# Kernel optimization log

Measured on AMD Instinct MI355X. Metric: run time of the kernel, lower is better.

## Reference

```python
import jax, jax.numpy as jnp
import numpy as np

N_NODES = 100000
N_EDGES = 1600000
D = 128
N_LAYERS = 4
N_GRAPHS = 512


def setup_inputs() -> dict:
    key = jax.random.key(0)
    ks = jax.random.split(key, 12)
    x = jax.random.normal(ks[0], (N_NODES, D), dtype=jnp.float32)
    edge_index = jax.random.randint(ks[1], (2, N_EDGES), 0, N_NODES, dtype=jnp.int64)
    batch = jnp.sort(jax.random.randint(ks[2], (N_NODES,), 0, N_GRAPHS, dtype=jnp.int64))
    scale = 1.0 / np.sqrt(D)
    Ws = jax.random.normal(ks[3], (N_LAYERS, D, D), dtype=jnp.float32) * scale
    bs = jnp.zeros((N_LAYERS, D), dtype=jnp.float32)
    mlp_w1 = jax.random.normal(ks[4], (D, 100), dtype=jnp.float32) * scale
    mlp_b1 = jnp.zeros((100,), dtype=jnp.float32)
    mlp_w2 = jax.random.normal(ks[5], (100, 4), dtype=jnp.float32) * (1.0 / np.sqrt(100.0))
    mlp_b2 = jnp.zeros((4,), dtype=jnp.float32)
    return {"x": x, "Ws": Ws, "bs": bs, "mlp_w1": mlp_w1, "mlp_b1": mlp_b1,
            "mlp_w2": mlp_w2, "mlp_b2": mlp_b2, "edge_index": edge_index, "batch": batch}


def _gcn_conv(x, W, b, row, col, norm):
    # x: [N, Din]; W: [Din, Dout]. PyG GCNConv: linear, then normalized scatter-add.
    xw = x @ W                                # [N, Dout]
    msg = xw[row] * norm[:, None]             # gather at source nodes [E', Dout]
    out = jax.ops.segment_sum(msg, col, num_segments=N_NODES)
    return out + b


def reference(x, Ws, bs, mlp_w1, mlp_b1, mlp_w2, mlp_b2, edge_index, batch):
    # Add self-loops and compute symmetric normalization (once; shared by all layers).
    loop = jnp.arange(N_NODES, dtype=edge_index.dtype)
    row = jnp.concatenate([edge_index[0], loop])  # source
    col = jnp.concatenate([edge_index[1], loop])  # target
    deg = jax.ops.segment_sum(jnp.ones_like(col, dtype=x.dtype), col, num_segments=N_NODES)
    dinv = jnp.where(deg > 0, jax.lax.rsqrt(deg), 0.0)
    norm = dinv[row] * dinv[col]              # [E']

    h = x
    for i in range(N_LAYERS - 1):
        # dropout is identity in eval mode
        h = _gcn_conv(h, Ws[i], bs[i], row, col, norm)
        h = jax.nn.relu(h)
    h = _gcn_conv(h, Ws[-1], bs[-1], row, col, norm)

    # global mean pool over graphs
    sums = jax.ops.segment_sum(h, batch, num_segments=N_GRAPHS)
    counts = jax.ops.segment_sum(jnp.ones((N_NODES,), dtype=h.dtype), batch, num_segments=N_GRAPHS)
    pooled = sums / jnp.maximum(counts, 1.0)[:, None]  # [G, D]

    # MLP head: D -> 100 -> 4 (relu between, dropout identity in eval)
    hid = jax.nn.relu(pooled @ mlp_w1 + mlp_b1)
    pred = hid @ mlp_w2 + mlp_b2
    return pred
```

## Files before the change

### kernel.cpp

```cpp
#include <hip/hip_runtime.h>

#define N_NODES  100000
#define N_EDGES  1600000
#define DIM      128
#define N_GRAPHS 512

#define BW       512
#define NBUCK    ((N_NODES + BW - 1) / BW)
#define CAP      12288
#define NB_CHUNK 4096

typedef short  bf16x8 __attribute__((ext_vector_type(8)));
typedef float  f32x4  __attribute__((ext_vector_type(4)));

__device__ inline ushort f2bf(float f) {
    union { float f; unsigned u; } v; v.f = f;
    unsigned r = v.u + 0x7FFFu + ((v.u >> 16) & 1u);
    return (ushort)(r >> 16);
}
__device__ inline float bf2f_lo(unsigned u) { union { unsigned u; float f; } v; v.u = u << 16; return v.f; }
__device__ inline float bf2f_hi(unsigned u) { union { unsigned u; float f; } v; v.u = u & 0xFFFF0000u; return v.f; }


__global__ __launch_bounds__(256) void cvt_x(const float* __restrict__ x,
                                             const float* __restrict__ dinv,
                                             ushort* __restrict__ xb) {
    int i = (blockIdx.x * 256 + threadIdx.x) * 4;
    float d = dinv[i >> 7];
    float4 v = *(const float4*)(x + i);
    ushort4 o;
    o.x = f2bf(v.x * d); o.y = f2bf(v.y * d); o.z = f2bf(v.z * d); o.w = f2bf(v.w * d);
    *(ushort4*)(xb + i) = o;
}

__global__ __launch_bounds__(256) void cvt_w(const float* __restrict__ Ws,
                                             ushort* __restrict__ WT) {
    int idx = blockIdx.x * 256 + threadIdx.x;
    int L = idx >> 14, n = (idx >> 7) & 127, k = idx & 127;
    WT[idx] = f2bf(Ws[(L << 14) + (k << 7) + n]);
}


__global__ __launch_bounds__(256) void initb_kernel(int* __restrict__ bfill,
                                                    int* __restrict__ csr) {
    int t = threadIdx.x;
    if (t < NBUCK) bfill[t] = t * CAP;
    if (t == 255) csr[N_NODES] = N_EDGES;
}

__global__ __launch_bounds__(1024) void bin_kernel(const int* __restrict__ row,
                                                   const int* __restrict__ col,
                                                   int* __restrict__ bfill,
                                                   unsigned* __restrict__ tmp) {
    __shared__ unsigned s_val[NB_CHUNK];
    __shared__ int s_dst[NB_CHUNK];
    __shared__ int s_hist[256], s_scan[256];
    __shared__ int s_excl[NBUCK], s_base[NBUCK], s_cur[NBUCK];
    int t = threadIdx.x;
    int e0 = blockIdx.x * NB_CHUNK;

    if (t < 256) s_hist[t] = 0;
    __syncthreads();
#pragma unroll
    for (int k = 0; k < 4; ++k) {
        int e = e0 + t + k * 1024;
        if (e < N_EDGES) atomicAdd(&s_hist[col[e] >> 9], 1);
    }
    __syncthreads();
    int h = 0;
    if (t < 256) { h = s_hist[t]; s_scan[t] = h; }
    __syncthreads();
    for (int o = 1; o < 256; o <<= 1) {
        int u = 0;
        if (t < 256 && t >= o) u = s_scan[t - o];
        __syncthreads();
        if (t < 256) s_scan[t] += u;
        __syncthreads();
    }
    if (t < NBUCK) {
        int ex = s_scan[t] - h;
        s_excl[t] = ex;
        s_cur[t]  = ex;
        s_base[t] = atomicAdd(&bfill[t], h);
    }
    __syncthreads();
#pragma unroll
    for (int k = 0; k < 4; ++k) {
        int e = e0 + t + k * 1024;
        if (e < N_EDGES) {
            int r = row[e], c = col[e];
            int b = c >> 9;
            int p = atomicAdd(&s_cur[b], 1);
            int dst = s_base[b] + (p - s_excl[b]);
            int lim = (b + 1) * CAP;
            if (dst >= lim) dst = lim - 1;
            s_val[p] = ((unsigned)(c & (BW - 1)) << 17) | (unsigned)r;
            s_dst[p] = dst;
        }
    }
    __syncthreads();
    int sc = N_EDGES - e0; if (sc > NB_CHUNK) sc = NB_CHUNK;
#pragma unroll
    for (int k = 0; k < 4; ++k) {
        int j = t + k * 1024;
        if (j < sc) tmp[s_dst[j]] = s_val[j];
    }
}

__global__ __launch_bounds__(256) void bscan_kernel(const int* __restrict__ bfill,
                                                    int* __restrict__ bbase) {
    __shared__ int s[256];
    int t = threadIdx.x;
    int cnt = 0;
    if (t < NBUCK) {
        cnt = bfill[t] - t * CAP;
        if (cnt > CAP) cnt = CAP;
    }
    s[t] = cnt;
    __syncthreads();
    for (int o = 1; o < 256; o <<= 1) {
        int u = (t >= o) ? s[t - o] : 0;
        __syncthreads();
        s[t] += u;
        __syncthreads();
    }
    if (t < NBUCK) bbase[t] = s[t] - cnt;
}

__global__ __launch_bounds__(1024) void sort_kernel(const unsigned* __restrict__ tmp,
                                                    const int* __restrict__ bfill,
                                                    const int* __restrict__ bbase,
                                                    int* __restrict__ csr,
                                                    float* __restrict__ dinv,
                                                    int* __restrict__ ssrc) {
    __shared__ int s_cnt[BW];
    __shared__ int s_pair[256];
    __shared__ int s_off[BW];
    __shared__ int s_cur[BW];
    __shared__ int s_stage[CAP];
    int b = blockIdx.x, t = threadIdx.x;
    int wbeg = b * BW;
    int wn = N_NODES - wbeg; if (wn > BW) wn = BW;
    int nE = bfill[b] - b * CAP; if (nE > CAP) nE = CAP;
    const unsigned* T = tmp + (size_t)b * CAP;
    int base = bbase[b];

    for (int i = t; i < BW; i += 1024) s_cnt[i] = 0;
    __syncthreads();
    for (int i = t; i < nE; i += 1024) atomicAdd(&s_cnt[T[i] >> 17], 1);
    __syncthreads();
    int a0 = 0, a1 = 0;
    if (t < 256) { a0 = s_cnt[2 * t]; a1 = s_cnt[2 * t + 1]; s_pair[t] = a0 + a1; }
    __syncthreads();
    for (int o = 1; o < 256; o <<= 1) {
        int u = 0;
        if (t < 256 && t >= o) u = s_pair[t - o];
        __syncthreads();
        if (t < 256) s_pair[t] += u;
        __syncthreads();
    }
    if (t < 256) {
        int pre = s_pair[t] - (a0 + a1);
        s_off[2 * t] = pre;      s_off[2 * t + 1] = pre + a0;
        s_cur[2 * t] = pre;      s_cur[2 * t + 1] = pre + a0;
    }
    __syncthreads();
    for (int i = t; i < wn; i += 1024) {
        csr[wbeg + i]  = base + s_off[i];
        dinv[wbeg + i] = rsqrtf((float)(s_cnt[i] + 1));
    }
    for (int i = t; i < nE; i += 1024) {
        unsigned v = T[i];
        int p = atomicAdd(&s_cur[v >> 17], 1);
        s_stage[p] = (int)(v & 0x1FFFFu);
    }
    __syncthreads();
    for (int i = t; i < nE; i += 1024) ssrc[base + i] = s_stage[i];
}

__global__ __launch_bounds__(256) void bounds_kernel(const int* __restrict__ batch,
                                                     int* __restrict__ gstart) {
    int i = blockIdx.x * 256 + threadIdx.x;
    if (i >= N_NODES) return;
    int b  = batch[i];
    int bp = (i == 0) ? -1 : batch[i - 1];
    for (int g = bp + 1; g <= b; ++g) gstart[g] = i;
    if (i == N_NODES - 1) {
        for (int g = b + 1; g <= N_GRAPHS; ++g) gstart[g] = N_NODES;
    }
}

#define ACC8(vv) do { \
    acc[0] += bf2f_lo((vv).x); acc[1] += bf2f_hi((vv).x); \
    acc[2] += bf2f_lo((vv).y); acc[3] += bf2f_hi((vv).y); \
    acc[4] += bf2f_lo((vv).z); acc[5] += bf2f_hi((vv).z); \
    acc[6] += bf2f_lo((vv).w); acc[7] += bf2f_hi((vv).w); } while (0)

__global__ __launch_bounds__(512) void layer_kernel(const ushort* __restrict__ g,
                                                    const ushort* __restrict__ WT,
                                                    const float* __restrict__ bias,
                                                    const float* __restrict__ dinv,
                                                    const int* __restrict__ csr,
                                                    const int* __restrict__ ssrc,
                                                    ushort* __restrict__ out,
                                                    int mode) {
    __shared__ ushort sW[128 * 128];
    __shared__ ushort sA[8][16 * 128];
    int t = threadIdx.x;
    int m0blk = blockIdx.x * 128;

    {
#pragma unroll
        for (int j = 0; j < 4; ++j) {
            int idx = t + j * 512;
            int r = idx >> 4, c = idx & 15;
            uint4 v = *(const uint4*)(WT + (size_t)r * 128 + c * 8);
            *(uint4*)(sW + r * 128 + ((c + r) & 15) * 8) = v;
        }
    }
    __syncthreads();

    int wv   = t >> 6;
    int lane = t & 63;
    int q    = lane >> 4;
    int l    = lane & 15;
    int mw   = m0blk + wv * 16;
    ushort* sAw = sA[wv];
    const uint4* hp = (const uint4*)g;

#pragma unroll 1
    for (int i = 0; i < 4; ++i) {
        int row  = q * 4 + i;
        int node = mw + row;
        float acc[8];
#pragma unroll
        for (int z = 0; z < 8; ++z) acc[z] = 0.f;
        if (node < N_NODES) {
            uint4 v = hp[(size_t)node * 16 + l];
            acc[0] = bf2f_lo(v.x); acc[1] = bf2f_hi(v.x);
            acc[2] = bf2f_lo(v.y); acc[3] = bf2f_hi(v.y);
            acc[4] = bf2f_lo(v.z); acc[5] = bf2f_hi(v.z);
            acc[6] = bf2f_lo(v.w); acc[7] = bf2f_hi(v.w);
            int e = csr[node], end = csr[node + 1];
            for (; e + 7 < end; e += 8) {
                int s0 = ssrc[e],     s1 = ssrc[e + 1], s2 = ssrc[e + 2], s3 = ssrc[e + 3];
                int s4 = ssrc[e + 4], s5 = ssrc[e + 5], s6 = ssrc[e + 6], s7 = ssrc[e + 7];
                uint4 v0 = hp[(size_t)s0 * 16 + l];
                uint4 v1 = hp[(size_t)s1 * 16 + l];
                uint4 v2 = hp[(size_t)s2 * 16 + l];
                uint4 v3 = hp[(size_t)s3 * 16 + l];
                uint4 v4 = hp[(size_t)s4 * 16 + l];
                uint4 v5 = hp[(size_t)s5 * 16 + l];
                uint4 v6 = hp[(size_t)s6 * 16 + l];
                uint4 v7 = hp[(size_t)s7 * 16 + l];
                ACC8(v0); ACC8(v1); ACC8(v2); ACC8(v3);
                ACC8(v4); ACC8(v5); ACC8(v6); ACC8(v7);
            }
            for (; e + 1 < end; e += 2) {
                int s0 = ssrc[e], s1 = ssrc[e + 1];
                uint4 v0 = hp[(size_t)s0 * 16 + l];
                uint4 v1 = hp[(size_t)s1 * 16 + l];
                ACC8(v0); ACC8(v1);
            }
            if (e < end) {
                int s = ssrc[e];
                uint4 v1 = hp[(size_t)s * 16 + l];
                ACC8(v1);
            }
            float d = dinv[node];
#pragma unroll
            for (int z = 0; z < 8; ++z) acc[z] *= d;
        }
        uint4 ov;
        ov.x = (uint)f2bf(acc[0]) | ((uint)f2bf(acc[1]) << 16);
        ov.y = (uint)f2bf(acc[2]) | ((uint)f2bf(acc[3]) << 16);
        ov.z = (uint)f2bf(acc[4]) | ((uint)f2bf(acc[5]) << 16);
        ov.w = (uint)f2bf(acc[6]) | ((uint)f2bf(acc[7]) << 16);
        *(uint4*)(sAw + row * 128 + ((l + row) & 15) * 8) = ov;
    }

    f32x4 facc[8];
#pragma unroll
    for (int n = 0; n < 8; ++n) facc[n] = (f32x4){0.f, 0.f, 0.f, 0.f};
#pragma unroll
    for (int ki = 0; ki < 4; ++ki) {
        int ca = ki * 4 + q;
        bf16x8 a = *(const bf16x8*)(sAw + l * 128 + ((ca + l) & 15) * 8);
#pragma unroll
        for (int n = 0; n < 8; ++n) {
            int rB = n * 16 + l;
            bf16x8 b = *(const bf16x8*)(sW + rB * 128 + ((ca + rB) & 15) * 8);
            facc[n] = __builtin_amdgcn_mfma_f32_16x16x32_bf16(a, b, facc[n], 0, 0, 0);
        }
    }

    {
        int lr0 = q * 4;
        float sc[4];
#pragma unroll
        for (int r = 0; r < 4; ++r) {
            int m = mw + lr0 + r;
            sc[r] = (mode && m < N_NODES) ? dinv[m] : 1.0f;
        }
#pragma unroll
        for (int n = 0; n < 8; ++n) {
            int col = n * 16 + l;
            float bv = bias[col];
            int c = col >> 3;
#pragma unroll
            for (int r = 0; r < 4; ++r) {
                int lr = lr0 + r;
                float v = facc[n][r] + bv;
                if (mode) v = fmaxf(v, 0.f) * sc[r];
                sAw[lr * 128 + ((c + lr) & 15) * 8 + (col & 7)] = f2bf(v);
            }
        }
    }
#pragma unroll
    for (int j = 0; j < 4; ++j) {
        int idx = lane + j * 64;
        int lr = idx >> 4, c = idx & 15;
        int m = mw + lr;
        if (m < N_NODES) {
            uint4 v = *(const uint4*)(sAw + lr * 128 + ((c + lr) & 15) * 8);
            *(uint4*)(out + (size_t)m * 128 + c * 8) = v;
        }
    }
}


__global__ __launch_bounds__(256) void pool_mlp(const ushort* __restrict__ h,
                                                const int* __restrict__ gstart,
                                                const float* __restrict__ w1,
                                                const float* __restrict__ b1,
                                                const float* __restrict__ w2,
                                                const float* __restrict__ b2,
                                                float* __restrict__ out) {
    __shared__ float part[4][128];
    __shared__ float mean[128];
    __shared__ float hid[100];
    int g = blockIdx.x;
    int s = gstart[g], e2 = gstart[g + 1];
    int p     = threadIdx.x & 63;
    int which = threadIdx.x >> 6;
    const uint* hu = (const uint*)h;

    float a0 = 0.f, a1 = 0.f;
    for (int n = s + which; n < e2; n += 4) {
        uint v = hu[(size_t)n * 64 + p];
        a0 += bf2f_lo(v);
        a1 += bf2f_hi(v);
    }
    part[which][2 * p]     = a0;
    part[which][2 * p + 1] = a1;
    __syncthreads();
    if (which == 0) {
        float c = fmaxf((float)(e2 - s), 1.0f);
        mean[2 * p]     = (part[0][2 * p] + part[1][2 * p] + part[2][2 * p] + part[3][2 * p]) / c;
        mean[2 * p + 1] = (part[0][2 * p + 1] + part[1][2 * p + 1] + part[2][2 * p + 1] + part[3][2 * p + 1]) / c;
    }
    __syncthreads();
    int t = threadIdx.x;
    if (t < 100) {
        float s1 = b1[t];
        for (int k = 0; k < 128; ++k) s1 = fmaf(mean[k], w1[k * 100 + t], s1);
        hid[t] = fmaxf(s1, 0.f);
    }
    __syncthreads();
    if (t < 4) {
        float s2 = b2[t];
        for (int j = 0; j < 100; ++j) s2 = fmaf(hid[j], w2[j * 4 + t], s2);
        out[(size_t)g * 4 + t] = s2;
    }
}


extern "C" void kernel_launch(void* const* d_in, const int* in_sizes, int n_in,
                              void* d_out, int out_size, void* d_ws, size_t ws_size,
                              hipStream_t stream) {
    const float* x   = (const float*)d_in[0];
    const float* Ws  = (const float*)d_in[1];
    const float* bs  = (const float*)d_in[2];
    const float* w1  = (const float*)d_in[3];
    const float* b1  = (const float*)d_in[4];
    const float* w2  = (const float*)d_in[5];
    const float* b2  = (const float*)d_in[6];
    const int*   ei  = (const int*)d_in[7];
    const int*   bat = (const int*)d_in[8];
    float* outp = (float*)d_out;

    char* p = (char*)d_ws;
    auto take = [&](size_t bytes) -> void* {
        void* r = (void*)p;
        p += (bytes + 255) & ~(size_t)255;
        return r;
    };
    int*      csr    = (int*)take((size_t)(N_NODES + 1) * 4);
    float*    dinv   = (float*)take((size_t)N_NODES * 4);
    int*      bfill  = (int*)take((size_t)NBUCK * 4);
    int*      bbase  = (int*)take((size_t)NBUCK * 4);
    unsigned* tmp    = (unsigned*)take((size_t)NBUCK * CAP * 4);
    int*      ssrc   = (int*)take((size_t)N_EDGES * 4);
    ushort*   xb     = (ushort*)take((size_t)N_NODES * 128 * 2);
    ushort*   hbA    = (ushort*)take((size_t)N_NODES * 128 * 2);
    ushort*   hbB    = (ushort*)take((size_t)N_NODES * 128 * 2);
    ushort*   WT     = (ushort*)take((size_t)4 * 128 * 128 * 2);
    int*      gstart = (int*)take((size_t)(N_GRAPHS + 1) * 4);

    const int* row = ei;
    const int* col = ei + N_EDGES;

    initb_kernel<<<1, 256, 0, stream>>>(bfill, csr);
    bin_kernel<<<(N_EDGES + NB_CHUNK - 1) / NB_CHUNK, 1024, 0, stream>>>(row, col, bfill, tmp);
    bscan_kernel<<<1, 256, 0, stream>>>(bfill, bbase);
    sort_kernel<<<NBUCK, 1024, 0, stream>>>(tmp, bfill, bbase, csr, dinv, ssrc);
    cvt_x<<<12500, 256, 0, stream>>>(x, dinv, xb);
    cvt_w<<<256, 256, 0, stream>>>(Ws, WT);
    bounds_kernel<<<(N_NODES + 255) / 256, 256, 0, stream>>>(bat, gstart);

    const ushort* hin = xb;
    ushort* hout = hbA;
    for (int L = 0; L < 4; ++L) {
        layer_kernel<<<(N_NODES + 127) / 128, 512, 0, stream>>>(
            hin, WT + (size_t)L * 128 * 128, bs + (size_t)L * 128, dinv,
            csr, ssrc, hout, (L < 3) ? 1 : 0);
        hin = hout;
        hout = (hout == hbA) ? hbB : hbA;
    }
    pool_mlp<<<N_GRAPHS, 256, 0, stream>>>(hin, gstart, w1, b1, w2, b2, outp);
}
```

Baseline: 457.4 us.

## Assign one wavefront per node for gather and split the MFMA across waves

The aggregation now uses a whole 64-lane wavefront per destination node, with each lane loading one 32-bit pair of bf16 values. Previously 16 lanes handled a node with 128-bit loads and four nodes ran in parallel per wave. Blocks shrink to 64 nodes, and the 64x128 tile is shared in LDS so that eight waves split the MFMA into row tiles and column halves, separated by block barriers. Launch bounds request more resident blocks to raise occupancy and latency hiding for the irregular gathers. The cost is more load instructions per byte and extra __syncthreads.

```diff
diff --git a/kernel.cpp b/kernel.cpp
--- a/kernel.cpp
+++ b/kernel.cpp
@@ -190,24 +190,18 @@
     }
 }
 
-#define ACC8(vv) do { \
-    acc[0] += bf2f_lo((vv).x); acc[1] += bf2f_hi((vv).x); \
-    acc[2] += bf2f_lo((vv).y); acc[3] += bf2f_hi((vv).y); \
-    acc[4] += bf2f_lo((vv).z); acc[5] += bf2f_hi((vv).z); \
-    acc[6] += bf2f_lo((vv).w); acc[7] += bf2f_hi((vv).w); } while (0)
-
-__global__ __launch_bounds__(512) void layer_kernel(const ushort* __restrict__ g,
-                                                    const ushort* __restrict__ WT,
-                                                    const float* __restrict__ bias,
-                                                    const float* __restrict__ dinv,
-                                                    const int* __restrict__ csr,
-                                                    const int* __restrict__ ssrc,
-                                                    ushort* __restrict__ out,
-                                                    int mode) {
+__global__ __launch_bounds__(512, 6) void layer_kernel(const ushort* __restrict__ g,
+                                                       const ushort* __restrict__ WT,
+                                                       const float* __restrict__ bias,
+                                                       const float* __restrict__ dinv,
+                                                       const int* __restrict__ csr,
+                                                       const int* __restrict__ ssrc,
+                                                       ushort* __restrict__ out,
+                                                       int mode) {
     __shared__ ushort sW[128 * 128];
-    __shared__ ushort sA[8][16 * 128];
+    __shared__ ushort sA[64 * 128];
     int t = threadIdx.x;
-    int m0blk = blockIdx.x * 128;
+    int m0 = blockIdx.x * 64;
 
     {
 #pragma unroll
@@ -218,111 +212,112 @@
             *(uint4*)(sW + r * 128 + ((c + r) & 15) * 8) = v;
         }
     }
-    __syncthreads();
-
-    int wv   = t >> 6;
+
+    int wv   = __builtin_amdgcn_readfirstlane(t >> 6);
     int lane = t & 63;
-    int q    = lane >> 4;
-    int l    = lane & 15;
-    int mw   = m0blk + wv * 16;
-    ushort* sAw = sA[wv];
-    const uint4* hp = (const uint4*)g;
+    const uint* hw = (const uint*)g;
 
 #pragma unroll 1
-    for (int i = 0; i < 4; ++i) {
-        int row  = q * 4 + i;
-        int node = mw + row;
-        float acc[8];
-#pragma unroll
-        for (int z = 0; z < 8; ++z) acc[z] = 0.f;
+    for (int i = 0; i < 8; ++i) {
+        int node = m0 + wv * 8 + i;
+        float a0 = 0.f, a1 = 0.f;
         if (node < N_NODES) {
-            uint4 v = hp[(size_t)node * 16 + l];
-            acc[0] = bf2f_lo(v.x); acc[1] = bf2f_hi(v.x);
-            acc[2] = bf2f_lo(v.y); acc[3] = bf2f_hi(v.y);
-            acc[4] = bf2f_lo(v.z); acc[5] = bf2f_hi(v.z);
-            acc[6] = bf2f_lo(v.w); acc[7] = bf2f_hi(v.w);
+            uint v = *(hw + (size_t)node * 64 + lane);
+            a0 = bf2f_lo(v); a1 = bf2f_hi(v);
             int e = csr[node], end = csr[node + 1];
+#pragma unroll 1
             for (; e + 7 < end; e += 8) {
                 int s0 = ssrc[e],     s1 = ssrc[e + 1], s2 = ssrc[e + 2], s3 = ssrc[e + 3];
                 int s4 = ssrc[e + 4], s5 = ssrc[e + 5], s6 = ssrc[e + 6], s7 = ssrc[e + 7];
-                uint4 v0 = hp[(size_t)s0 * 16 + l];
-                uint4 v1 = hp[(size_t)s1 * 16 + l];
-                uint4 v2 = hp[(size_t)s2 * 16 + l];
-                uint4 v3 = hp[(size_t)s3 * 16 + l];
-                uint4 v4 = hp[(size_t)s4 * 16 + l];
-                uint4 v5 = hp[(size_t)s5 * 16 + l];
-                uint4 v6 = hp[(size_t)s6 * 16 + l];
-                uint4 v7 = hp[(size_t)s7 * 16 + l];
-                ACC8(v0); ACC8(v1); ACC8(v2); ACC8(v3);
-                ACC8(v4); ACC8(v5); ACC8(v6); ACC8(v7);
+                uint v0 = *(hw + (size_t)s0 * 64 + lane);
+                uint v1 = *(hw + (size_t)s1 * 64 + lane);
+                uint v2 = *(hw + (size_t)s2 * 64 + lane);
+                uint v3 = *(hw + (size_t)s3 * 64 + lane);
+                uint v4 = *(hw + (size_t)s4 * 64 + lane);
+                uint v5 = *(hw + (size_t)s5 * 64 + lane);
+                uint v6 = *(hw + (size_t)s6 * 64 + lane);
+                uint v7 = *(hw + (size_t)s7 * 64 + lane);
+                a0 += bf2f_lo(v0); a1 += bf2f_hi(v0);
+                a0 += bf2f_lo(v1); a1 += bf2f_hi(v1);
+                a0 += bf2f_lo(v2); a1 += bf2f_hi(v2);
+                a0 += bf2f_lo(v3); a1 += bf2f_hi(v3);
+                a0 += bf2f_lo(v4); a1 += bf2f_hi(v4);
+                a0 += bf2f_lo(v5); a1 += bf2f_hi(v5);
+                a0 += bf2f_lo(v6); a1 += bf2f_hi(v6);
+                a0 += bf2f_lo(v7); a1 += bf2f_hi(v7);
             }
+#pragma unroll 1
             for (; e + 1 < end; e += 2) {
                 int s0 = ssrc[e], s1 = ssrc[e + 1];
-                uint4 v0 = hp[(size_t)s0 * 16 + l];
-                uint4 v1 = hp[(size_t)s1 * 16 + l];
-                ACC8(v0); ACC8(v1);
+                uint v0 = *(hw + (size_t)s0 * 64 + lane);
+                uint v1 = *(hw + (size_t)s1 * 64 + lane);
+                a0 += bf2f_lo(v0); a1 += bf2f_hi(v0);
+                a0 += bf2f_lo(v1); a1 += bf2f_hi(v1);
             }
             if (e < end) {
-                int s = ssrc[e];
-                uint4 v1 = hp[(size_t)s * 16 + l];
-                ACC8(v1);
+                uint v0 = *(hw + (size_t)ssrc[e] * 64 + lane);
+                a0 += bf2f_lo(v0); a1 += bf2f_hi(v0);
             }
             float d = dinv[node];
-#pragma unroll
-            for (int z = 0; z < 8; ++z) acc[z] *= d;
-        }
-        uint4 ov;
-        ov.x = (uint)f2bf(acc[0]) | ((uint)f2bf(acc[1]) << 16);
-        ov.y = (uint)f2bf(acc[2]) | ((uint)f2bf(acc[3]) << 16);
-        ov.z = (uint)f2bf(acc[4]) | ((uint)f2bf(acc[5]) << 16);
-        ov.w = (uint)f2bf(acc[6]) | ((uint)f2bf(acc[7]) << 16);
-        *(uint4*)(sAw + row * 128 + ((l + row) & 15) * 8) = ov;
-    }
-
-    f32x4 facc[8];
-#pragma unroll
-    for (int n = 0; n < 8; ++n) facc[n] = (f32x4){0.f, 0.f, 0.f, 0.f};
+            a0 *= d; a1 *= d;
+        }
+        int r = wv * 8 + i;
+        uint wo = (uint)f2bf(a0) | ((uint)f2bf(a1) << 16);
+        ((uint*)sA)[r * 64 + (((lane >> 2) + r) & 15) * 4 + (lane & 3)] = wo;
+    }
+    __syncthreads();
+
+    int rt = wv >> 1;
+    int ch = wv & 1;
+    int q  = lane >> 4;
+    int l  = lane & 15;
+    f32x4 facc[4];
+#pragma unroll
+    for (int n = 0; n < 4; ++n) facc[n] = (f32x4){0.f, 0.f, 0.f, 0.f};
 #pragma unroll
     for (int ki = 0; ki < 4; ++ki) {
         int ca = ki * 4 + q;
-        bf16x8 a = *(const bf16x8*)(sAw + l * 128 + ((ca + l) & 15) * 8);
-#pragma unroll
-        for (int n = 0; n < 8; ++n) {
-            int rB = n * 16 + l;
+        int ra = rt * 16 + l;
+        bf16x8 a = *(const bf16x8*)(sA + ra * 128 + ((ca + ra) & 15) * 8);
+#pragma unroll
+        for (int n = 0; n < 4; ++n) {
+            int rB = ch * 64 + n * 16 + l;
             bf16x8 b = *(const bf16x8*)(sW + rB * 128 + ((ca + rB) & 15) * 8);
             facc[n] = __builtin_amdgcn_mfma_f32_16x16x32_bf16(a, b, facc[n], 0, 0, 0);
         }
     }
+    __syncthreads();
 
     {
-        int lr0 = q * 4;
+        int lr0 = rt * 16 + q * 4;
         float sc[4];
 #pragma unroll
-        for (int r = 0; r < 4; ++r) {
-            int m = mw + lr0 + r;
-            sc[r] = (mode && m < N_NODES) ? dinv[m] : 1.0f;
-        }
-#pragma unroll
-        for (int n = 0; n < 8; ++n) {
-            int col = n * 16 + l;
+        for (int r2 = 0; r2 < 4; ++r2) {
+            int m = m0 + lr0 + r2;
+            sc[r2] = (mode && m < N_NODES) ? dinv[m] : 1.0f;
+        }
+#pragma unroll
+        for (int n = 0; n < 4; ++n) {
+            int col = ch * 64 + n * 16 + l;
             float bv = bias[col];
             int c = col >> 3;
 #pragma unroll
-            for (int r = 0; r < 4; ++r) {
-                int lr = lr0 + r;
-                float v = facc[n][r] + bv;
-                if (mode) v = fmaxf(v, 0.f) * sc[r];
-                sAw[lr * 128 + ((c + lr) & 15) * 8 + (col & 7)] = f2bf(v);
+            for (int r2 = 0; r2 < 4; ++r2) {
+                int lr = lr0 + r2;
+                float v = facc[n][r2] + bv;
+                if (mode) v = fmaxf(v, 0.f) * sc[r2];
+                sA[lr * 128 + ((c + lr) & 15) * 8 + (col & 7)] = f2bf(v);
             }
         }
     }
-#pragma unroll
-    for (int j = 0; j < 4; ++j) {
-        int idx = lane + j * 64;
+    __syncthreads();
+#pragma unroll
+    for (int j = 0; j < 2; ++j) {
+        int idx = t + j * 512;
         int lr = idx >> 4, c = idx & 15;
-        int m = mw + lr;
+        int m = m0 + lr;
         if (m < N_NODES) {
-            uint4 v = *(const uint4*)(sAw + lr * 128 + ((c + lr) & 15) * 8);
+            uint4 v = *(const uint4*)(sA + lr * 128 + ((c + lr) & 15) * 8);
             *(uint4*)(out + (size_t)m * 128 + c * 8) = v;
         }
     }
@@ -421,7 +416,7 @@
     const ushort* hin = xb;
     ushort* hout = hbA;
     for (int L = 0; L < 4; ++L) {
-        layer_kernel<<<(N_NODES + 127) / 128, 512, 0, stream>>>(
+        layer_kernel<<<(N_NODES + 63) / 64, 512, 0, stream>>>(
             hin, WT + (size_t)L * 128 * 128, bs + (size_t)L * 128, dinv,
             csr, ssrc, hout, (L < 3) ? 1 : 0);
         hin = hout;
```

Result: slower. 468.6 us (+2.5%).
